# Optimization experiments

Measured on AMD Instinct MI355X. Metric: run time of the kernel, lower is better.

## Reference

```python
import jax, jax.numpy as jnp
import numpy as np

B, L, S, H, E = 2, 2048, 2048, 8, 64
MASK_SCALE = 10000.0
TAU_MIN, TAU_MAX = 0.1, 5.0
THR_MIN, THR_MAX = 0.01, 0.99


def setup_inputs() -> dict:
    key = jax.random.key(0)
    ks = jax.random.split(key, 7)
    query = jax.random.normal(ks[0], (B, L, H, E), jnp.float32)
    k_ = jax.random.normal(ks[1], (B, S, H, E), jnp.float32)
    value = jax.random.normal(ks[2], (B, S, H, E), jnp.float32)
    mask_miss_k = jnp.zeros((B, S), jnp.float32)  # unused in forward
    mask_miss_q = jnp.zeros((B, L), jnp.float32)  # unused in forward
    pos = jnp.arange(B * L, dtype=jnp.int32).reshape(B, L, 1)  # monotone positions per batch
    hard_mask = jax.random.randint(ks[3], (L, S), 0, 2, dtype=jnp.int32)
    hard_mask = hard_mask.at[jnp.arange(L), jnp.arange(S)].set(1)  # keep diagonal open
    # learned parameters / stochastic state
    phi = jax.random.normal(ks[4], (H, L, S), jnp.float32)  # DAG edge logits (per head)
    log_tau_gs = jnp.asarray(np.log(2.0), jnp.float32)
    threshold = jnp.asarray(0.5, jnp.float32)
    u = jax.random.uniform(ks[5], (H, L, S), jnp.float32, 1e-6, 1.0 - 1e-6)  # Gumbel base noise
    return {"query": query, "key": k_, "value": value, "mask_miss_k": mask_miss_k,
            "mask_miss_q": mask_miss_q, "pos": pos, "causal_mask": 1,
            "hard_mask": hard_mask, "phi": phi, "log_tau_gs": log_tau_gs,
            "threshold": threshold, "u": u}


def reference(query, key, value, mask_miss_k, mask_miss_q, pos, causal_mask,
              hard_mask, phi, log_tau_gs, threshold, u):
    e = query.shape[-1]
    scale = 1.0 / np.sqrt(e)
    # scores: (B, H, L, S)
    scores = jnp.einsum('blhe,bshe->bhls', query, key)
    if causal_mask:
        p = pos[..., 0]  # (B, L)
        causal = jnp.where(p[:, None, :] > p[:, :, None], -jnp.inf, 0.0).astype(scores.dtype)
        scores = scores + causal[:, None, :, :]
    # Gumbel-sigmoid relaxed DAG mask
    tau = jnp.clip(jnp.exp(log_tau_gs), TAU_MIN, TAU_MAX)
    gumbel = jnp.log(u + 1e-8) - jnp.log(1.0 - u + 1e-8)
    m_relaxed = jax.nn.sigmoid((gumbel + phi) / tau)  # (H, L, S)
    thr = jnp.clip(threshold, THR_MIN, THR_MAX)
    dag_add = MASK_SCALE * jnp.minimum(m_relaxed - thr, 0.0)  # <=0 additive penalty
    scores = scores + dag_add[None, :, :, :]
    # hard mask applied pre-softmax as -inf
    scores = jnp.where(hard_mask[None, None, :, :] == 0, -jnp.inf, scores)
    att = jax.nn.softmax(scale * scores, axis=-1)  # dropout p=0 (eval)
    out = jnp.einsum('bhls,bshe->blhe', att, value)  # (B, L, H, E)
    return out
```

## Files before the change

kernel.cpp:

```cpp
#include <hip/hip_runtime.h>


#define Bz 2
#define Lz 2048
#define Sz 2048
#define Hz 8
#define Ez 64
#define NSEG 4
#define NEG_BIG (-1e30f)

typedef __attribute__((ext_vector_type(8))) short short8;
typedef __attribute__((ext_vector_type(4))) short short4v;
typedef __attribute__((ext_vector_type(4))) float f32x4;

__device__ __forceinline__ float fast_rcp(float x) { return __builtin_amdgcn_rcpf(x); }

__device__ __forceinline__ short f2bf(float x) {
    unsigned bits = __builtin_bit_cast(unsigned, x);
    bits += 0x7FFFu + ((bits >> 16) & 1u);
    return (short)(bits >> 16);
}

__global__ void pack_qk(const float* __restrict__ q, const float* __restrict__ k,
                        short* __restrict__ qp, short* __restrict__ kp)
{
    const int t = blockIdx.x * 256 + threadIdx.x;
    const float4 qv = ((const float4*)q)[t];
    const float4 kv = ((const float4*)k)[t];
    const int e4   = t & 15;
    const int rest = t >> 4;
    const int h    = rest & 7;
    const int bl   = rest >> 3;
    const int b    = bl >> 11;
    const int l    = bl & 2047;
    const int o    = ((b*Hz + h)*Lz + l)*Ez + e4*4;
    short4v qo, ko;
    qo[0] = f2bf(qv.x*0.125f); qo[1] = f2bf(qv.y*0.125f);
    qo[2] = f2bf(qv.z*0.125f); qo[3] = f2bf(qv.w*0.125f);
    ko[0] = f2bf(kv.x); ko[1] = f2bf(kv.y); ko[2] = f2bf(kv.z); ko[3] = f2bf(kv.w);
    *(short4v*)&qp[o] = qo;
    *(short4v*)&kp[o] = ko;
}

__global__ void pack_vt(const float* __restrict__ v, short* __restrict__ vt)
{
    const int blk = blockIdx.x;
    const int st  = blk & 63;
    const int h   = (blk >> 6) & 7;
    const int b   = blk >> 9;
    const int s0  = st * 32;
    const int e   = threadIdx.x & 63;
    const int sc  = threadIdx.x >> 6;
    short8 ov;
#pragma unroll
    for (int j = 0; j < 8; ++j) {
        const int s = s0 + sc*8 + j;
        ov[j] = f2bf(v[((b*Sz + s)*Hz + h)*Ez + e]);
    }
    *(short8*)&vt[((b*Hz + h)*Ez + e)*Sz + s0 + sc*8] = ov;
}

__global__ __launch_bounds__(256, 2) void attn_main(
    const float* __restrict__ phi, const float* __restrict__ u,
    const int* __restrict__ hard_mask, const int* __restrict__ causal_p,
    const float* __restrict__ log_tau_p, const float* __restrict__ thr_p,
    const short* __restrict__ qp, const short* __restrict__ kp,
    const short* __restrict__ vt,
    float* __restrict__ Op, float* __restrict__ Mp, float* __restrict__ Lp)
{
    const int lane  = threadIdx.x & 63;
    const int wslot = threadIdx.x >> 6;
    const int wu    = blockIdx.x * 4 + wslot;
    const int seg   = wu & 3;
    const int qq    = wu >> 2;
    const int h     = qq & 7;
    const int c     = 127 - (qq >> 3);
    const int l_base = c * 16;
    const int ln    = lane & 15;
    const int quad  = lane >> 4;

    const int causal = *causal_p;
    float tau = __expf(*log_tau_p);
    tau = fminf(fmaxf(tau, 0.1f), 5.0f);
    const float inv_tau = 1.0f / tau;
    const float thr = fminf(fmaxf(*thr_p, 0.01f), 0.99f);

    short8 qf[2][2];
#pragma unroll
    for (int b = 0; b < 2; ++b)
#pragma unroll
        for (int k = 0; k < 2; ++k)
            qf[b][k] = *(const short8*)&qp[((b*Hz + h)*Lz + l_base + ln)*Ez + k*32 + quad*8];

    f32x4 O[2][4];
    float m_r[2][4], l_r[2][4];
#pragma unroll
    for (int b = 0; b < 2; ++b) {
#pragma unroll
        for (int ne = 0; ne < 4; ++ne) { f32x4 z = {0.f,0.f,0.f,0.f}; O[b][ne] = z; }
#pragma unroll
        for (int r = 0; r < 4; ++r) { m_r[b][r] = -INFINITY; l_r[b][r] = 0.f; }
    }

    const int T = causal ? (((l_base + 15) >> 6) + 1) : (Sz >> 6);

    __shared__ __align__(16) short plds[4][16*72];
    short* myp = &plds[wslot][0];

    for (int t = seg; t < T; t += NSEG) {
        const int s0 = t << 6;

        float dg[4][4];
#pragma unroll
        for (int nt = 0; nt < 4; ++nt) {
#pragma unroll
            for (int r = 0; r < 4; ++r) {
                const int l = l_base + quad*4 + r;
                const int s = s0 + nt*16 + ln;
                const int off = (h*Lz + l)*Sz + s;
                const float ph = phi[off];
                const float uv = u[off];
                const int   hm = hard_mask[l*Sz + s];
                const float g  = __logf((uv + 1e-8f) * fast_rcp(1.0f - uv + 1e-8f));
                const float z  = (g + ph) * inv_tau;
                const float sg = fast_rcp(1.0f + __expf(-z));
                const float d  = 1250.0f * fminf(sg - thr, 0.0f);
                const bool dead = (hm == 0) || (causal && (s > l));
                dg[nt][r] = dead ? -INFINITY : d;
            }
        }

#pragma unroll
        for (int b = 0; b < 2; ++b) {
            short8 kf[4][2];
#pragma unroll
            for (int nt = 0; nt < 4; ++nt)
#pragma unroll
                for (int k = 0; k < 2; ++k)
                    kf[nt][k] = *(const short8*)&kp[((b*Hz + h)*Sz + s0 + nt*16 + ln)*Ez + k*32 + quad*8];

            f32x4 Sc[4];
#pragma unroll
            for (int nt = 0; nt < 4; ++nt) {
                f32x4 z4 = {0.f,0.f,0.f,0.f};
                z4 = __builtin_amdgcn_mfma_f32_16x16x32_bf16(qf[b][0], kf[nt][0], z4, 0, 0, 0);
                Sc[nt] = __builtin_amdgcn_mfma_f32_16x16x32_bf16(qf[b][1], kf[nt][1], z4, 0, 0, 0);
            }

            float tv[4][4], mx[4];
#pragma unroll
            for (int r = 0; r < 4; ++r) mx[r] = -INFINITY;
#pragma unroll
            for (int nt = 0; nt < 4; ++nt)
#pragma unroll
                for (int r = 0; r < 4; ++r) {
                    const float val = Sc[nt][r] + dg[nt][r];
                    tv[nt][r] = val;
                    mx[r] = fmaxf(mx[r], val);
                }
#pragma unroll
            for (int r = 0; r < 4; ++r)
#pragma unroll
                for (int o = 1; o < 16; o <<= 1)
                    mx[r] = fmaxf(mx[r], __shfl_xor(mx[r], o, 16));

            float al[4], mn[4];
#pragma unroll
            for (int r = 0; r < 4; ++r) {
                mn[r] = fmaxf(m_r[b][r], mx[r]);
                al[r] = __expf(fmaxf(m_r[b][r], NEG_BIG) - fmaxf(mn[r], NEG_BIG));
                m_r[b][r] = mn[r];
            }

            float ps[4] = {0.f, 0.f, 0.f, 0.f};
#pragma unroll
            for (int nt = 0; nt < 4; ++nt)
#pragma unroll
                for (int r = 0; r < 4; ++r) {
                    const float p = __expf(tv[nt][r] - fmaxf(mn[r], NEG_BIG));
                    ps[r] += p;
                    myp[(quad*4 + r)*72 + nt*16 + ln] = f2bf(p);
                }
#pragma unroll
            for (int r = 0; r < 4; ++r) {
#pragma unroll
                for (int o = 1; o < 16; o <<= 1)
                    ps[r] += __shfl_xor(ps[r], o, 16);
                l_r[b][r] = l_r[b][r] * al[r] + ps[r];
            }
#pragma unroll
            for (int ne = 0; ne < 4; ++ne)
#pragma unroll
                for (int r = 0; r < 4; ++r)
                    O[b][ne][r] *= al[r];

            short8 pa[2];
#pragma unroll
            for (int k = 0; k < 2; ++k)
                pa[k] = *(const short8*)&myp[ln*72 + k*32 + quad*8];

#pragma unroll
            for (int ne = 0; ne < 4; ++ne) {
                const short8 v0 = *(const short8*)&vt[((b*Hz + h)*Ez + ne*16 + ln)*Sz + s0 + quad*8];
                const short8 v1 = *(const short8*)&vt[((b*Hz + h)*Ez + ne*16 + ln)*Sz + s0 + 32 + quad*8];
                O[b][ne] = __builtin_amdgcn_mfma_f32_16x16x32_bf16(pa[0], v0, O[b][ne], 0, 0, 0);
                O[b][ne] = __builtin_amdgcn_mfma_f32_16x16x32_bf16(pa[1], v1, O[b][ne], 0, 0, 0);
            }
        }
    }

#pragma unroll
    for (int b = 0; b < 2; ++b) {
#pragma unroll
        for (int ne = 0; ne < 4; ++ne)
#pragma unroll
            for (int r = 0; r < 4; ++r) {
                const int l = l_base + quad*4 + r;
                Op[(((seg*2 + b)*Hz + h)*Lz + l)*Ez + ne*16 + ln] = O[b][ne][r];
            }
        if (ln == 0) {
#pragma unroll
            for (int r = 0; r < 4; ++r) {
                const int l = l_base + quad*4 + r;
                Mp[((seg*2 + b)*Hz + h)*Lz + l] = m_r[b][r];
                Lp[((seg*2 + b)*Hz + h)*Lz + l] = l_r[b][r];
            }
        }
    }
}

__global__ void merge_k(const float* __restrict__ Op, const float* __restrict__ Mp,
                        const float* __restrict__ Lp, float* __restrict__ out)
{
    const int t = blockIdx.x * 256 + threadIdx.x;
    const int e4   = (t & 15) * 4;
    const int rest = t >> 4;
    const int h    = rest & 7;
    const int bl   = rest >> 3;
    const int b    = bl >> 11;
    const int l    = bl & 2047;

    float ms[NSEG], ls[NSEG], m = -INFINITY;
#pragma unroll
    for (int s = 0; s < NSEG; ++s) {
        const int idx = ((s*2 + b)*Hz + h)*Lz + l;
        ms[s] = Mp[idx];
        ls[s] = Lp[idx];
        m = fmaxf(m, ms[s]);
    }
    const float mg = fmaxf(m, NEG_BIG);
    float den = 0.f, a0 = 0.f, a1 = 0.f, a2 = 0.f, a3 = 0.f;
#pragma unroll
    for (int s = 0; s < NSEG; ++s) {
        const float w = __expf(fmaxf(ms[s], NEG_BIG) - mg);
        den += w * ls[s];
        const float4 ov = *(const float4*)&Op[(((s*2 + b)*Hz + h)*Lz + l)*Ez + e4];
        a0 += w * ov.x; a1 += w * ov.y; a2 += w * ov.z; a3 += w * ov.w;
    }
    const float rd = 1.0f / den;
    float4 res;
    res.x = a0 * rd; res.y = a1 * rd; res.z = a2 * rd; res.w = a3 * rd;
    *(float4*)&out[((b*Lz + l)*Hz + h)*Ez + e4] = res;
}

extern "C" void kernel_launch(void* const* d_in, const int* in_sizes, int n_in,
                              void* d_out, int out_size, void* d_ws, size_t ws_size,
                              hipStream_t stream)
{
    const float* q     = (const float*)d_in[0];
    const float* k     = (const float*)d_in[1];
    const float* v     = (const float*)d_in[2];
    const int*   caus  = (const int*)d_in[6];
    const int*   hm    = (const int*)d_in[7];
    const float* phi   = (const float*)d_in[8];
    const float* ltau  = (const float*)d_in[9];
    const float* thr   = (const float*)d_in[10];
    const float* u     = (const float*)d_in[11];

    char* ws = (char*)d_ws;
    short* qp = (short*)(ws);
    short* kp = (short*)(ws + (size_t)( 4u << 20));
    short* vt = (short*)(ws + (size_t)( 8u << 20));
    float* Op = (float*)(ws + (size_t)(12u << 20));
    float* Mp = (float*)(ws + (size_t)(44u << 20));
    float* Lp = (float*)(ws + (size_t)(44u << 20) + (512u << 10));

    pack_qk <<<2048, 256, 0, stream>>>(q, k, qp, kp);
    pack_vt <<<1024, 256, 0, stream>>>(v, vt);
    attn_main<<<1024, 256, 0, stream>>>(phi, u, hm, caus, ltau, thr, qp, kp, vt, Op, Mp, Lp);
    merge_k <<<2048, 256, 0, stream>>>(Op, Mp, Lp, (float*)d_out);
}
```

Baseline: 400.1 us.

## Split KV into 8 segments with in-block merge, bitpacked hard mask, prefetched phi/u

Raises the KV split from 4 to 8 segments per query tile and doubles the grid. Each block's four waves now combine their partials in shared memory, so only two partials per row reach global memory and the final merge reads half as much. The hard mask is packed into bits in a new pre-pass, and phi/u loads for the next tile are double-buffered into registers to hide their latency. The per-tile row-sum shuffles move to a single reduction after the loop. The cost is more register pressure from the prefetch buffers, an extra kernel launch, and extra shared memory plus a block barrier.

```diff
diff --git a/kernel.cpp b/kernel.cpp
--- a/kernel.cpp
+++ b/kernel.cpp
@@ -6,7 +6,6 @@
 #define Sz 2048
 #define Hz 8
 #define Ez 64
-#define NSEG 4
 #define NEG_BIG (-1e30f)
 
 typedef __attribute__((ext_vector_type(8))) short short8;
@@ -60,24 +59,40 @@
     *(short8*)&vt[((b*Hz + h)*Ez + e)*Sz + s0 + sc*8] = ov;
 }
 
+__global__ void pack_hm(const int* __restrict__ hm, unsigned* __restrict__ hmb)
+{
+    const int t = blockIdx.x * 256 + threadIdx.x;
+    const int4* src = (const int4*)hm + t*8;
+    unsigned w = 0;
+#pragma unroll
+    for (int i = 0; i < 8; ++i) {
+        const int4 v = src[i];
+        w |= (v.x != 0 ? 1u : 0u) << (i*4 + 0);
+        w |= (v.y != 0 ? 1u : 0u) << (i*4 + 1);
+        w |= (v.z != 0 ? 1u : 0u) << (i*4 + 2);
+        w |= (v.w != 0 ? 1u : 0u) << (i*4 + 3);
+    }
+    hmb[t] = w;
+}
+
 __global__ __launch_bounds__(256, 2) void attn_main(
     const float* __restrict__ phi, const float* __restrict__ u,
-    const int* __restrict__ hard_mask, const int* __restrict__ causal_p,
+    const unsigned* __restrict__ hmb, const int* __restrict__ causal_p,
     const float* __restrict__ log_tau_p, const float* __restrict__ thr_p,
     const short* __restrict__ qp, const short* __restrict__ kp,
     const short* __restrict__ vt,
-    float* __restrict__ Op, float* __restrict__ Mp, float* __restrict__ Lp)
-{
-    const int lane  = threadIdx.x & 63;
-    const int wslot = threadIdx.x >> 6;
-    const int wu    = blockIdx.x * 4 + wslot;
-    const int seg   = wu & 3;
-    const int qq    = wu >> 2;
-    const int h     = qq & 7;
-    const int c     = 127 - (qq >> 3);
-    const int l_base = c * 16;
-    const int ln    = lane & 15;
-    const int quad  = lane >> 4;
+    float* __restrict__ Og, float* __restrict__ Mg, float* __restrict__ Lg)
+{
+    const int lane    = threadIdx.x & 63;
+    const int wslot   = threadIdx.x >> 6;
+    const int h       = blockIdx.x & 7;
+    const int r2      = blockIdx.x >> 3;
+    const int segpair = r2 & 1;
+    const int c       = 127 - (r2 >> 1);
+    const int seg     = segpair*4 + wslot;
+    const int l_base  = c * 16;
+    const int ln      = lane & 15;
+    const int quad    = lane >> 4;
 
     const int causal = *causal_p;
     float tau = __expf(*log_tau_p);
@@ -104,59 +119,66 @@
 
     const int T = causal ? (((l_base + 15) >> 6) + 1) : (Sz >> 6);
 
-    __shared__ __align__(16) short plds[4][16*72];
-    short* myp = &plds[wslot][0];
-
-    for (int t = seg; t < T; t += NSEG) {
+    __shared__ __align__(16) short plds[4][2][16*72];
+
+    const int mbase = (h*Lz + l_base + quad*4)*Sz + ln;
+
+    auto ldmask = [&](int t, float (&P)[16], float (&U)[16]) {
+        const int o0 = mbase + (t << 6);
+#pragma unroll
+        for (int nt = 0; nt < 4; ++nt)
+#pragma unroll
+            for (int r = 0; r < 4; ++r) {
+                P[nt*4+r] = phi[o0 + r*Sz + nt*16];
+                U[nt*4+r] = u[o0 + r*Sz + nt*16];
+            }
+    };
+
+    auto process = [&](int t, const float (&P)[16], const float (&U)[16]) {
         const int s0 = t << 6;
-
-        float dg[4][4];
-#pragma unroll
-        for (int nt = 0; nt < 4; ++nt) {
+        unsigned long long hmr[4];
+#pragma unroll
+        for (int r = 0; r < 4; ++r)
+            hmr[r] = *(const unsigned long long*)&hmb[(l_base + quad*4 + r)*64 + (s0 >> 5)];
+
+        float dg[16];
+#pragma unroll
+        for (int nt = 0; nt < 4; ++nt)
 #pragma unroll
             for (int r = 0; r < 4; ++r) {
                 const int l = l_base + quad*4 + r;
                 const int s = s0 + nt*16 + ln;
-                const int off = (h*Lz + l)*Sz + s;
-                const float ph = phi[off];
-                const float uv = u[off];
-                const int   hm = hard_mask[l*Sz + s];
+                const float uv = U[nt*4+r];
                 const float g  = __logf((uv + 1e-8f) * fast_rcp(1.0f - uv + 1e-8f));
-                const float z  = (g + ph) * inv_tau;
+                const float z  = (g + P[nt*4+r]) * inv_tau;
                 const float sg = fast_rcp(1.0f + __expf(-z));
                 const float d  = 1250.0f * fminf(sg - thr, 0.0f);
-                const bool dead = (hm == 0) || (causal && (s > l));
-                dg[nt][r] = dead ? -INFINITY : d;
-            }
-        }
+                const bool open = (((hmr[r] >> (nt*16 + ln)) & 1ull) != 0ull)
+                                  && !(causal && (s > l));
+                dg[nt*4+r] = open ? d : -INFINITY;
+            }
 
 #pragma unroll
         for (int b = 0; b < 2; ++b) {
-            short8 kf[4][2];
+            f32x4 Sc[4];
+#pragma unroll
+            for (int nt = 0; nt < 4; ++nt) {
+                const short8 k0 = *(const short8*)&kp[((b*Hz + h)*Sz + s0 + nt*16 + ln)*Ez + quad*8];
+                const short8 k1 = *(const short8*)&kp[((b*Hz + h)*Sz + s0 + nt*16 + ln)*Ez + 32 + quad*8];
+                f32x4 z4 = {0.f,0.f,0.f,0.f};
+                z4 = __builtin_amdgcn_mfma_f32_16x16x32_bf16(qf[b][0], k0, z4, 0, 0, 0);
+                Sc[nt] = __builtin_amdgcn_mfma_f32_16x16x32_bf16(qf[b][1], k1, Sc[nt] = z4, 0, 0, 0);
+            }
+
+            float mx[4];
+#pragma unroll
+            for (int r = 0; r < 4; ++r) mx[r] = -INFINITY;
 #pragma unroll
             for (int nt = 0; nt < 4; ++nt)
 #pragma unroll
-                for (int k = 0; k < 2; ++k)
-                    kf[nt][k] = *(const short8*)&kp[((b*Hz + h)*Sz + s0 + nt*16 + ln)*Ez + k*32 + quad*8];
-
-            f32x4 Sc[4];
-#pragma unroll
-            for (int nt = 0; nt < 4; ++nt) {
-                f32x4 z4 = {0.f,0.f,0.f,0.f};
-                z4 = __builtin_amdgcn_mfma_f32_16x16x32_bf16(qf[b][0], kf[nt][0], z4, 0, 0, 0);
-                Sc[nt] = __builtin_amdgcn_mfma_f32_16x16x32_bf16(qf[b][1], kf[nt][1], z4, 0, 0, 0);
-            }
-
-            float tv[4][4], mx[4];
-#pragma unroll
-            for (int r = 0; r < 4; ++r) mx[r] = -INFINITY;
-#pragma unroll
-            for (int nt = 0; nt < 4; ++nt)
-#pragma unroll
                 for (int r = 0; r < 4; ++r) {
-                    const float val = Sc[nt][r] + dg[nt][r];
-                    tv[nt][r] = val;
-                    mx[r] = fmaxf(mx[r], val);
+                    Sc[nt][r] += dg[nt*4+r];
+                    mx[r] = fmaxf(mx[r], Sc[nt][r]);
                 }
 #pragma unroll
             for (int r = 0; r < 4; ++r)
@@ -164,73 +186,127 @@
                 for (int o = 1; o < 16; o <<= 1)
                     mx[r] = fmaxf(mx[r], __shfl_xor(mx[r], o, 16));
 
-            float al[4], mn[4];
+            float al[4];
 #pragma unroll
             for (int r = 0; r < 4; ++r) {
-                mn[r] = fmaxf(m_r[b][r], mx[r]);
-                al[r] = __expf(fmaxf(m_r[b][r], NEG_BIG) - fmaxf(mn[r], NEG_BIG));
-                m_r[b][r] = mn[r];
-            }
-
+                const float mn = fmaxf(m_r[b][r], mx[r]);
+                al[r] = __expf(fmaxf(m_r[b][r], NEG_BIG) - fmaxf(mn, NEG_BIG));
+                m_r[b][r] = mn;
+            }
+
+            short* myp = &plds[wslot][b][0];
             float ps[4] = {0.f, 0.f, 0.f, 0.f};
 #pragma unroll
             for (int nt = 0; nt < 4; ++nt)
 #pragma unroll
                 for (int r = 0; r < 4; ++r) {
-                    const float p = __expf(tv[nt][r] - fmaxf(mn[r], NEG_BIG));
+                    const float p = __expf(Sc[nt][r] - fmaxf(m_r[b][r], NEG_BIG));
                     ps[r] += p;
                     myp[(quad*4 + r)*72 + nt*16 + ln] = f2bf(p);
                 }
 #pragma unroll
-            for (int r = 0; r < 4; ++r) {
-#pragma unroll
-                for (int o = 1; o < 16; o <<= 1)
-                    ps[r] += __shfl_xor(ps[r], o, 16);
+            for (int r = 0; r < 4; ++r)
                 l_r[b][r] = l_r[b][r] * al[r] + ps[r];
-            }
 #pragma unroll
             for (int ne = 0; ne < 4; ++ne)
 #pragma unroll
                 for (int r = 0; r < 4; ++r)
                     O[b][ne][r] *= al[r];
 
-            short8 pa[2];
-#pragma unroll
-            for (int k = 0; k < 2; ++k)
-                pa[k] = *(const short8*)&myp[ln*72 + k*32 + quad*8];
-
+            const short8 pa0 = *(const short8*)&myp[ln*72 + quad*8];
+            const short8 pa1 = *(const short8*)&myp[ln*72 + 32 + quad*8];
 #pragma unroll
             for (int ne = 0; ne < 4; ++ne) {
                 const short8 v0 = *(const short8*)&vt[((b*Hz + h)*Ez + ne*16 + ln)*Sz + s0 + quad*8];
                 const short8 v1 = *(const short8*)&vt[((b*Hz + h)*Ez + ne*16 + ln)*Sz + s0 + 32 + quad*8];
-                O[b][ne] = __builtin_amdgcn_mfma_f32_16x16x32_bf16(pa[0], v0, O[b][ne], 0, 0, 0);
-                O[b][ne] = __builtin_amdgcn_mfma_f32_16x16x32_bf16(pa[1], v1, O[b][ne], 0, 0, 0);
+                O[b][ne] = __builtin_amdgcn_mfma_f32_16x16x32_bf16(pa0, v0, O[b][ne], 0, 0, 0);
+                O[b][ne] = __builtin_amdgcn_mfma_f32_16x16x32_bf16(pa1, v1, O[b][ne], 0, 0, 0);
             }
         }
-    }
-
+    };
+
+    float PA[16], UA[16], PB[16], UB[16];
+    int t = seg;
+    if (t < T) ldmask(t, PA, UA);
+    int parity = 0;
+    for (; t < T; t += 8, parity ^= 1) {
+        if (parity == 0) {
+            if (t + 8 < T) ldmask(t + 8, PB, UB);
+            process(t, PA, UA);
+        } else {
+            if (t + 8 < T) ldmask(t + 8, PA, UA);
+            process(t, PB, UB);
+        }
+    }
+
+#pragma unroll
+    for (int b = 0; b < 2; ++b)
+#pragma unroll
+        for (int r = 0; r < 4; ++r) {
+            float lv = l_r[b][r];
+#pragma unroll
+            for (int o = 1; o < 16; o <<= 1) lv += __shfl_xor(lv, o, 16);
+            l_r[b][r] = lv;
+        }
+
+    __shared__ float oslab[4][2][16][64];
+    __shared__ float mslab[4][2][16];
+    __shared__ float lslab[4][2][16];
 #pragma unroll
     for (int b = 0; b < 2; ++b) {
 #pragma unroll
         for (int ne = 0; ne < 4; ++ne)
 #pragma unroll
+            for (int r = 0; r < 4; ++r)
+                oslab[wslot][b][quad*4 + r][ne*16 + ln] = O[b][ne][r];
+        if (ln == 0) {
+#pragma unroll
             for (int r = 0; r < 4; ++r) {
-                const int l = l_base + quad*4 + r;
-                Op[(((seg*2 + b)*Hz + h)*Lz + l)*Ez + ne*16 + ln] = O[b][ne][r];
-            }
-        if (ln == 0) {
-#pragma unroll
-            for (int r = 0; r < 4; ++r) {
-                const int l = l_base + quad*4 + r;
-                Mp[((seg*2 + b)*Hz + h)*Lz + l] = m_r[b][r];
-                Lp[((seg*2 + b)*Hz + h)*Lz + l] = l_r[b][r];
+                mslab[wslot][b][quad*4 + r] = m_r[b][r];
+                lslab[wslot][b][quad*4 + r] = l_r[b][r];
             }
         }
     }
-}
-
-__global__ void merge_k(const float* __restrict__ Op, const float* __restrict__ Mp,
-                        const float* __restrict__ Lp, float* __restrict__ out)
+    __syncthreads();
+
+    const int tb   = threadIdx.x >> 7;
+    const int trow = (threadIdx.x >> 3) & 15;
+    const int teg  = threadIdx.x & 7;
+    float mM = -INFINITY;
+#pragma unroll
+    for (int w = 0; w < 4; ++w) mM = fmaxf(mM, mslab[w][tb][trow]);
+    const float mMg = fmaxf(mM, NEG_BIG);
+    float wgt[4]; float lsum = 0.f;
+#pragma unroll
+    for (int w = 0; w < 4; ++w) {
+        wgt[w] = __expf(fmaxf(mslab[w][tb][trow], NEG_BIG) - mMg);
+        lsum += wgt[w] * lslab[w][tb][trow];
+    }
+    float acc[8];
+#pragma unroll
+    for (int e = 0; e < 8; ++e) acc[e] = 0.f;
+#pragma unroll
+    for (int w = 0; w < 4; ++w)
+#pragma unroll
+        for (int e = 0; e < 8; ++e)
+            acc[e] += wgt[w] * oslab[w][tb][trow][teg*8 + e];
+
+    const int lrow = l_base + trow;
+    const int oidx = (((segpair*2 + tb)*Hz + h)*Lz + lrow)*Ez + teg*8;
+    float4 o0, o1;
+    o0.x = acc[0]; o0.y = acc[1]; o0.z = acc[2]; o0.w = acc[3];
+    o1.x = acc[4]; o1.y = acc[5]; o1.z = acc[6]; o1.w = acc[7];
+    *(float4*)&Og[oidx]     = o0;
+    *(float4*)&Og[oidx + 4] = o1;
+    if (teg == 0) {
+        const int midx = ((segpair*2 + tb)*Hz + h)*Lz + lrow;
+        Mg[midx] = mM;
+        Lg[midx] = lsum;
+    }
+}
+
+__global__ void merge2(const float* __restrict__ Og, const float* __restrict__ Mg,
+                       const float* __restrict__ Lg, float* __restrict__ out)
 {
     const int t = blockIdx.x * 256 + threadIdx.x;
     const int e4   = (t & 15) * 4;
@@ -240,26 +316,23 @@
     const int b    = bl >> 11;
     const int l    = bl & 2047;
 
-    float ms[NSEG], ls[NSEG], m = -INFINITY;
-#pragma unroll
-    for (int s = 0; s < NSEG; ++s) {
-        const int idx = ((s*2 + b)*Hz + h)*Lz + l;
-        ms[s] = Mp[idx];
-        ls[s] = Lp[idx];
-        m = fmaxf(m, ms[s]);
-    }
+    const int i0 = ((0*2 + b)*Hz + h)*Lz + l;
+    const int i1 = ((1*2 + b)*Hz + h)*Lz + l;
+    const float m0 = Mg[i0], m1 = Mg[i1];
+    const float l0 = Lg[i0], l1 = Lg[i1];
+    const float m  = fmaxf(m0, m1);
     const float mg = fmaxf(m, NEG_BIG);
-    float den = 0.f, a0 = 0.f, a1 = 0.f, a2 = 0.f, a3 = 0.f;
-#pragma unroll
-    for (int s = 0; s < NSEG; ++s) {
-        const float w = __expf(fmaxf(ms[s], NEG_BIG) - mg);
-        den += w * ls[s];
-        const float4 ov = *(const float4*)&Op[(((s*2 + b)*Hz + h)*Lz + l)*Ez + e4];
-        a0 += w * ov.x; a1 += w * ov.y; a2 += w * ov.z; a3 += w * ov.w;
-    }
-    const float rd = 1.0f / den;
+    const float w0 = __expf(fmaxf(m0, NEG_BIG) - mg);
+    const float w1 = __expf(fmaxf(m1, NEG_BIG) - mg);
+    const float den = w0*l0 + w1*l1;
+    const float rd  = 1.0f / den;
+    const float4 a = *(const float4*)&Og[i0*Ez + e4];
+    const float4 c = *(const float4*)&Og[i1*Ez + e4];
     float4 res;
-    res.x = a0 * rd; res.y = a1 * rd; res.z = a2 * rd; res.w = a3 * rd;
+    res.x = (w0*a.x + w1*c.x) * rd;
+    res.y = (w0*a.y + w1*c.y) * rd;
+    res.z = (w0*a.z + w1*c.z) * rd;
+    res.w = (w0*a.w + w1*c.w) * rd;
     *(float4*)&out[((b*Lz + l)*Hz + h)*Ez + e4] = res;
 }
 
@@ -267,26 +340,28 @@
                               void* d_out, int out_size, void* d_ws, size_t ws_size,
                               hipStream_t stream)
 {
-    const float* q     = (const float*)d_in[0];
-    const float* k     = (const float*)d_in[1];
-    const float* v     = (const float*)d_in[2];
-    const int*   caus  = (const int*)d_in[6];
-    const int*   hm    = (const int*)d_in[7];
-    const float* phi   = (const float*)d_in[8];
-    const float* ltau  = (const float*)d_in[9];
-    const float* thr   = (const float*)d_in[10];
-    const float* u     = (const float*)d_in[11];
+    const float* q    = (const float*)d_in[0];
+    const float* k    = (const float*)d_in[1];
+    const float* v    = (const float*)d_in[2];
+    const int*   caus = (const int*)d_in[6];
+    const int*   hm   = (const int*)d_in[7];
+    const float* phi  = (const float*)d_in[8];
+    const float* ltau = (const float*)d_in[9];
+    const float* thr  = (const float*)d_in[10];
+    const float* u    = (const float*)d_in[11];
 
     char* ws = (char*)d_ws;
-    short* qp = (short*)(ws);
-    short* kp = (short*)(ws + (size_t)( 4u << 20));
-    short* vt = (short*)(ws + (size_t)( 8u << 20));
-    float* Op = (float*)(ws + (size_t)(12u << 20));
-    float* Mp = (float*)(ws + (size_t)(44u << 20));
-    float* Lp = (float*)(ws + (size_t)(44u << 20) + (512u << 10));
+    short*    qp  = (short*)   (ws);
+    short*    kp  = (short*)   (ws + (size_t)( 4u << 20));
+    short*    vt  = (short*)   (ws + (size_t)( 8u << 20));
+    unsigned* hmb = (unsigned*)(ws + (size_t)(12u << 20));
+    float*    Og  = (float*)   (ws + (size_t)(13u << 20));
+    float*    Mg  = (float*)   (ws + (size_t)(29u << 20));
+    float*    Lg  = (float*)   (ws + (size_t)(29u << 20) + (256u << 10));
 
     pack_qk <<<2048, 256, 0, stream>>>(q, k, qp, kp);
     pack_vt <<<1024, 256, 0, stream>>>(v, vt);
-    attn_main<<<1024, 256, 0, stream>>>(phi, u, hm, caus, ltau, thr, qp, kp, vt, Op, Mp, Lp);
-    merge_k <<<2048, 256, 0, stream>>>(Op, Mp, Lp, (float*)d_out);
-}
+    pack_hm <<< 512, 256, 0, stream>>>(hm, hmb);
+    attn_main<<<2048, 256, 0, stream>>>(phi, u, hmb, caus, ltau, thr, qp, kp, vt, Og, Mg, Lg);
+    merge2  <<<2048, 256, 0, stream>>>(Og, Mg, Lg, (float*)d_out);
+}
```

Result: no change. 404.4 us (+1.1%).

## Precompute bf16 DAG mask with row-max shift, drop online softmax and merge kernel

Applied to the files above, without the earlier changes.

Adds a mask kernel that computes the Gumbel-sigmoid DAG penalty once per (h,l,s), takes its row maximum over open entries, and stores the shifted penalty as bf16 in a causal-packed tile layout. Because QK scores are tiny next to the penalty scale, the attention kernel uses this fixed shift as a stable max and skips online-softmax rescaling. It also splits the key range across 8 waves of one block per (b,h,chunk) and merges them in shared memory, so the separate merge kernel and its partial-output traffic go away. The costs are two passes over phi/u in the mask kernel, a bf16 round-trip for the penalty, and reliance on scores staying small for exp to stay in range.

```diff
diff --git a/kernel.cpp b/kernel.cpp
--- a/kernel.cpp
+++ b/kernel.cpp
@@ -6,8 +6,6 @@
 #define Sz 2048
 #define Hz 8
 #define Ez 64
-#define NSEG 4
-#define NEG_BIG (-1e30f)
 
 typedef __attribute__((ext_vector_type(8))) short short8;
 typedef __attribute__((ext_vector_type(4))) short short4v;
@@ -19,6 +17,12 @@
     unsigned bits = __builtin_bit_cast(unsigned, x);
     bits += 0x7FFFu + ((bits >> 16) & 1u);
     return (short)(bits >> 16);
+}
+
+__device__ __forceinline__ int tile_base_of_chunk(int c, int causal) {
+    if (!causal) return c * 32;
+    const int g = c >> 2, r = c & 3;
+    return 2*g*(g-1) + g*r + c;
 }
 
 __global__ void pack_qk(const float* __restrict__ q, const float* __restrict__ k,
@@ -60,233 +64,219 @@
     *(short8*)&vt[((b*Hz + h)*Ez + e)*Sz + s0 + sc*8] = ov;
 }
 
-__global__ __launch_bounds__(256, 2) void attn_main(
+__global__ __launch_bounds__(256) void mask_k(
     const float* __restrict__ phi, const float* __restrict__ u,
-    const int* __restrict__ hard_mask, const int* __restrict__ causal_p,
+    const int* __restrict__ hm, const int* __restrict__ causal_p,
     const float* __restrict__ log_tau_p, const float* __restrict__ thr_p,
-    const short* __restrict__ qp, const short* __restrict__ kp,
-    const short* __restrict__ vt,
-    float* __restrict__ Op, float* __restrict__ Mp, float* __restrict__ Lp)
-{
-    const int lane  = threadIdx.x & 63;
-    const int wslot = threadIdx.x >> 6;
-    const int wu    = blockIdx.x * 4 + wslot;
-    const int seg   = wu & 3;
-    const int qq    = wu >> 2;
-    const int h     = qq & 7;
-    const int c     = 127 - (qq >> 3);
-    const int l_base = c * 16;
-    const int ln    = lane & 15;
-    const int quad  = lane >> 4;
-
+    unsigned short* __restrict__ dag)
+{
+    const int h = blockIdx.x & 7;
+    const int c = 127 - (blockIdx.x >> 3);
     const int causal = *causal_p;
     float tau = __expf(*log_tau_p);
     tau = fminf(fmaxf(tau, 0.1f), 5.0f);
     const float inv_tau = 1.0f / tau;
     const float thr = fminf(fmaxf(*thr_p, 0.01f), 0.99f);
 
-    short8 qf[2][2];
-#pragma unroll
-    for (int b = 0; b < 2; ++b)
-#pragma unroll
-        for (int k = 0; k < 2; ++k)
-            qf[b][k] = *(const short8*)&qp[((b*Hz + h)*Lz + l_base + ln)*Ez + k*32 + quad*8];
-
-    f32x4 O[2][4];
-    float m_r[2][4], l_r[2][4];
-#pragma unroll
-    for (int b = 0; b < 2; ++b) {
-#pragma unroll
-        for (int ne = 0; ne < 4; ++ne) { f32x4 z = {0.f,0.f,0.f,0.f}; O[b][ne] = z; }
-#pragma unroll
-        for (int r = 0; r < 4; ++r) { m_r[b][r] = -INFINITY; l_r[b][r] = 0.f; }
-    }
-
-    const int T = causal ? (((l_base + 15) >> 6) + 1) : (Sz >> 6);
-
-    __shared__ __align__(16) short plds[4][16*72];
-    short* myp = &plds[wslot][0];
-
-    for (int t = seg; t < T; t += NSEG) {
-        const int s0 = t << 6;
-
-        float dg[4][4];
+    const int T   = causal ? ((c >> 2) + 1) : 32;
+    const int row = threadIdx.x >> 4;
+    const int sc4 = (threadIdx.x & 15) * 4;
+    const int l   = c*16 + row;
+    const float* prow = &phi[(h*Lz + l)*Sz];
+    const float* urow = &u[(h*Lz + l)*Sz];
+    const int*   hrow = &hm[l*Sz];
+
+    float md = -INFINITY;
+    for (int t = 0; t < T; ++t) {
+        const int s = t*64 + sc4;
+        const float4 ph = *(const float4*)&prow[s];
+        const float4 uv = *(const float4*)&urow[s];
+        const int4   hv = *(const int4*)&hrow[s];
+        const float pa[4] = {ph.x, ph.y, ph.z, ph.w};
+        const float ua[4] = {uv.x, uv.y, uv.z, uv.w};
+        const int   ha[4] = {hv.x, hv.y, hv.z, hv.w};
+#pragma unroll
+        for (int j = 0; j < 4; ++j) {
+            const float g  = __logf((ua[j] + 1e-8f) * fast_rcp(1.0f - ua[j] + 1e-8f));
+            const float z  = (g + pa[j]) * inv_tau;
+            const float sg = fast_rcp(1.0f + __expf(-z));
+            const float d  = 1250.0f * fminf(sg - thr, 0.0f);
+            const bool open = (ha[j] != 0) && !(causal && (s + j > l));
+            if (open) md = fmaxf(md, d);
+        }
+    }
+#pragma unroll
+    for (int o = 1; o < 16; o <<= 1)
+        md = fmaxf(md, __shfl_xor(md, o, 16));
+
+    const int hstride = causal ? 2112 : 4096;
+    unsigned short* dbase = dag + (h*hstride + tile_base_of_chunk(c, causal))*1024
+                                + row*64 + sc4;
+    for (int t = T - 1; t >= 0; --t) {
+        const int s = t*64 + sc4;
+        const float4 ph = *(const float4*)&prow[s];
+        const float4 uv = *(const float4*)&urow[s];
+        const int4   hv = *(const int4*)&hrow[s];
+        const float pa[4] = {ph.x, ph.y, ph.z, ph.w};
+        const float ua[4] = {uv.x, uv.y, uv.z, uv.w};
+        const int   ha[4] = {hv.x, hv.y, hv.z, hv.w};
+        unsigned short o4[4];
+#pragma unroll
+        for (int j = 0; j < 4; ++j) {
+            const float g  = __logf((ua[j] + 1e-8f) * fast_rcp(1.0f - ua[j] + 1e-8f));
+            const float z  = (g + pa[j]) * inv_tau;
+            const float sg = fast_rcp(1.0f + __expf(-z));
+            const float d  = 1250.0f * fminf(sg - thr, 0.0f);
+            const bool open = (ha[j] != 0) && !(causal && (s + j > l));
+            o4[j] = open ? (unsigned short)f2bf(d - md) : (unsigned short)0xFF80u;
+        }
+        unsigned short* dst = dbase + t*1024;
+        dst[0] = o4[0]; dst[1] = o4[1]; dst[2] = o4[2]; dst[3] = o4[3];
+    }
+}
+
+__global__ __launch_bounds__(512, 4) void attn_main(
+    const unsigned short* __restrict__ dag, const int* __restrict__ causal_p,
+    const short* __restrict__ qp, const short* __restrict__ kp,
+    const short* __restrict__ vt, float* __restrict__ out)
+{
+    const int lane = threadIdx.x & 63;
+    const int seg  = threadIdx.x >> 6;
+    const int h    = blockIdx.x & 7;
+    const int b    = (blockIdx.x >> 3) & 1;
+    const int c    = 127 - (blockIdx.x >> 4);
+    const int l_base = c * 16;
+    const int ln   = lane & 15;
+    const int quad = lane >> 4;
+
+    const int causal = *causal_p;
+    const int T = causal ? ((c >> 2) + 1) : 32;
+    const int hstride = causal ? 2112 : 4096;
+    const unsigned short* dbase = dag + (h*hstride + tile_base_of_chunk(c, causal))*1024
+                                      + (quad*4)*64 + ln;
+
+    short8 qf[2];
+#pragma unroll
+    for (int k = 0; k < 2; ++k)
+        qf[k] = *(const short8*)&qp[((b*Hz + h)*Lz + l_base + ln)*Ez + k*32 + quad*8];
+
+    f32x4 O[4];
+    float l_r[4];
+#pragma unroll
+    for (int ne = 0; ne < 4; ++ne) { f32x4 z = {0.f,0.f,0.f,0.f}; O[ne] = z; }
+#pragma unroll
+    for (int r = 0; r < 4; ++r) l_r[r] = 0.f;
+
+    __shared__ __align__(16) char shm[8 * 4608];
+    __shared__ float lslab[8][16];
+    short* myp = (short*)(shm + seg*4608);
+
+    auto lddag = [&](int t, unsigned (&D)[16]) {
+        const unsigned short* dp = dbase + t*1024;
+#pragma unroll
+        for (int nt = 0; nt < 4; ++nt)
+#pragma unroll
+            for (int r = 0; r < 4; ++r)
+                D[nt*4+r] = dp[r*64 + nt*16];
+    };
+
+    auto process = [&](int t, const unsigned (&D)[16]) {
+        const short* kbase = &kp[((b*Hz + h)*Sz + t*64 + ln)*Ez + quad*8];
+        f32x4 Sc[4];
 #pragma unroll
         for (int nt = 0; nt < 4; ++nt) {
+            const short8 k0 = *(const short8*)&kbase[nt*16*Ez];
+            const short8 k1 = *(const short8*)&kbase[nt*16*Ez + 32];
+            f32x4 z4 = {0.f,0.f,0.f,0.f};
+            z4 = __builtin_amdgcn_mfma_f32_16x16x32_bf16(qf[0], k0, z4, 0, 0, 0);
+            Sc[nt] = __builtin_amdgcn_mfma_f32_16x16x32_bf16(qf[1], k1, z4, 0, 0, 0);
+        }
+#pragma unroll
+        for (int nt = 0; nt < 4; ++nt)
 #pragma unroll
             for (int r = 0; r < 4; ++r) {
-                const int l = l_base + quad*4 + r;
-                const int s = s0 + nt*16 + ln;
-                const int off = (h*Lz + l)*Sz + s;
-                const float ph = phi[off];
-                const float uv = u[off];
-                const int   hm = hard_mask[l*Sz + s];
-                const float g  = __logf((uv + 1e-8f) * fast_rcp(1.0f - uv + 1e-8f));
-                const float z  = (g + ph) * inv_tau;
-                const float sg = fast_rcp(1.0f + __expf(-z));
-                const float d  = 1250.0f * fminf(sg - thr, 0.0f);
-                const bool dead = (hm == 0) || (causal && (s > l));
-                dg[nt][r] = dead ? -INFINITY : d;
+                const float dg = __builtin_bit_cast(float, D[nt*4+r] << 16);
+                const float p  = __expf(Sc[nt][r] + dg);
+                l_r[r] += p;
+                myp[(quad*4 + r)*72 + nt*16 + ln] = f2bf(p);
             }
-        }
-
-#pragma unroll
-        for (int b = 0; b < 2; ++b) {
-            short8 kf[4][2];
-#pragma unroll
-            for (int nt = 0; nt < 4; ++nt)
-#pragma unroll
-                for (int k = 0; k < 2; ++k)
-                    kf[nt][k] = *(const short8*)&kp[((b*Hz + h)*Sz + s0 + nt*16 + ln)*Ez + k*32 + quad*8];
-
-            f32x4 Sc[4];
-#pragma unroll
-            for (int nt = 0; nt < 4; ++nt) {
-                f32x4 z4 = {0.f,0.f,0.f,0.f};
-                z4 = __builtin_amdgcn_mfma_f32_16x16x32_bf16(qf[b][0], kf[nt][0], z4, 0, 0, 0);
-                Sc[nt] = __builtin_amdgcn_mfma_f32_16x16x32_bf16(qf[b][1], kf[nt][1], z4, 0, 0, 0);
-            }
-
-            float tv[4][4], mx[4];
-#pragma unroll
-            for (int r = 0; r < 4; ++r) mx[r] = -INFINITY;
-#pragma unroll
-            for (int nt = 0; nt < 4; ++nt)
-#pragma unroll
-                for (int r = 0; r < 4; ++r) {
-                    const float val = Sc[nt][r] + dg[nt][r];
-                    tv[nt][r] = val;
-                    mx[r] = fmaxf(mx[r], val);
-                }
-#pragma unroll
-            for (int r = 0; r < 4; ++r)
-#pragma unroll
-                for (int o = 1; o < 16; o <<= 1)
-                    mx[r] = fmaxf(mx[r], __shfl_xor(mx[r], o, 16));
-
-            float al[4], mn[4];
-#pragma unroll
-            for (int r = 0; r < 4; ++r) {
-                mn[r] = fmaxf(m_r[b][r], mx[r]);
-                al[r] = __expf(fmaxf(m_r[b][r], NEG_BIG) - fmaxf(mn[r], NEG_BIG));
-                m_r[b][r] = mn[r];
-            }
-
-            float ps[4] = {0.f, 0.f, 0.f, 0.f};
-#pragma unroll
-            for (int nt = 0; nt < 4; ++nt)
-#pragma unroll
-                for (int r = 0; r < 4; ++r) {
-                    const float p = __expf(tv[nt][r] - fmaxf(mn[r], NEG_BIG));
-                    ps[r] += p;
-                    myp[(quad*4 + r)*72 + nt*16 + ln] = f2bf(p);
-                }
-#pragma unroll
-            for (int r = 0; r < 4; ++r) {
-#pragma unroll
-                for (int o = 1; o < 16; o <<= 1)
-                    ps[r] += __shfl_xor(ps[r], o, 16);
-                l_r[b][r] = l_r[b][r] * al[r] + ps[r];
-            }
-#pragma unroll
-            for (int ne = 0; ne < 4; ++ne)
-#pragma unroll
-                for (int r = 0; r < 4; ++r)
-                    O[b][ne][r] *= al[r];
-
-            short8 pa[2];
-#pragma unroll
-            for (int k = 0; k < 2; ++k)
-                pa[k] = *(const short8*)&myp[ln*72 + k*32 + quad*8];
-
-#pragma unroll
-            for (int ne = 0; ne < 4; ++ne) {
-                const short8 v0 = *(const short8*)&vt[((b*Hz + h)*Ez + ne*16 + ln)*Sz + s0 + quad*8];
-                const short8 v1 = *(const short8*)&vt[((b*Hz + h)*Ez + ne*16 + ln)*Sz + s0 + 32 + quad*8];
-                O[b][ne] = __builtin_amdgcn_mfma_f32_16x16x32_bf16(pa[0], v0, O[b][ne], 0, 0, 0);
-                O[b][ne] = __builtin_amdgcn_mfma_f32_16x16x32_bf16(pa[1], v1, O[b][ne], 0, 0, 0);
-            }
-        }
-    }
-
-#pragma unroll
-    for (int b = 0; b < 2; ++b) {
-#pragma unroll
-        for (int ne = 0; ne < 4; ++ne)
-#pragma unroll
-            for (int r = 0; r < 4; ++r) {
-                const int l = l_base + quad*4 + r;
-                Op[(((seg*2 + b)*Hz + h)*Lz + l)*Ez + ne*16 + ln] = O[b][ne][r];
-            }
-        if (ln == 0) {
-#pragma unroll
-            for (int r = 0; r < 4; ++r) {
-                const int l = l_base + quad*4 + r;
-                Mp[((seg*2 + b)*Hz + h)*Lz + l] = m_r[b][r];
-                Lp[((seg*2 + b)*Hz + h)*Lz + l] = l_r[b][r];
-            }
-        }
-    }
-}
-
-__global__ void merge_k(const float* __restrict__ Op, const float* __restrict__ Mp,
-                        const float* __restrict__ Lp, float* __restrict__ out)
-{
-    const int t = blockIdx.x * 256 + threadIdx.x;
-    const int e4   = (t & 15) * 4;
-    const int rest = t >> 4;
-    const int h    = rest & 7;
-    const int bl   = rest >> 3;
-    const int b    = bl >> 11;
-    const int l    = bl & 2047;
-
-    float ms[NSEG], ls[NSEG], m = -INFINITY;
-#pragma unroll
-    for (int s = 0; s < NSEG; ++s) {
-        const int idx = ((s*2 + b)*Hz + h)*Lz + l;
-        ms[s] = Mp[idx];
-        ls[s] = Lp[idx];
-        m = fmaxf(m, ms[s]);
-    }
-    const float mg = fmaxf(m, NEG_BIG);
-    float den = 0.f, a0 = 0.f, a1 = 0.f, a2 = 0.f, a3 = 0.f;
-#pragma unroll
-    for (int s = 0; s < NSEG; ++s) {
-        const float w = __expf(fmaxf(ms[s], NEG_BIG) - mg);
-        den += w * ls[s];
-        const float4 ov = *(const float4*)&Op[(((s*2 + b)*Hz + h)*Lz + l)*Ez + e4];
-        a0 += w * ov.x; a1 += w * ov.y; a2 += w * ov.z; a3 += w * ov.w;
+        const short8 pa0 = *(const short8*)&myp[ln*72 + quad*8];
+        const short8 pa1 = *(const short8*)&myp[ln*72 + 32 + quad*8];
+        const short* vb = &vt[((b*Hz + h)*Ez + ln)*Sz + t*64 + quad*8];
+#pragma unroll
+        for (int ne = 0; ne < 4; ++ne) {
+            const short8 v0 = *(const short8*)&vb[ne*16*Sz];
+            const short8 v1 = *(const short8*)&vb[ne*16*Sz + 32];
+            O[ne] = __builtin_amdgcn_mfma_f32_16x16x32_bf16(pa0, v0, O[ne], 0, 0, 0);
+            O[ne] = __builtin_amdgcn_mfma_f32_16x16x32_bf16(pa1, v1, O[ne], 0, 0, 0);
+        }
+    };
+
+    unsigned DA[16], DB[16];
+    int t = seg;
+    if (t < T) lddag(t, DA);
+    int parity = 0;
+    for (; t < T; t += 8, parity ^= 1) {
+        if (!parity) { if (t + 8 < T) lddag(t + 8, DB); process(t, DA); }
+        else         { if (t + 8 < T) lddag(t + 8, DA); process(t, DB); }
+    }
+
+#pragma unroll
+    for (int r = 0; r < 4; ++r) {
+        float lv = l_r[r];
+#pragma unroll
+        for (int o = 1; o < 16; o <<= 1) lv += __shfl_xor(lv, o, 16);
+        l_r[r] = lv;
+    }
+    float* fo = (float*)(shm + seg*4608);
+#pragma unroll
+    for (int ne = 0; ne < 4; ++ne)
+#pragma unroll
+        for (int r = 0; r < 4; ++r)
+            fo[(quad*4 + r)*64 + ne*16 + ln] = O[ne][r];
+    if (ln == 0) {
+#pragma unroll
+        for (int r = 0; r < 4; ++r) lslab[seg][quad*4 + r] = l_r[r];
+    }
+    __syncthreads();
+
+    const int row = threadIdx.x >> 5;
+    const int e   = (threadIdx.x & 31) * 2;
+    float den = 0.f, a0 = 0.f, a1 = 0.f;
+#pragma unroll
+    for (int w = 0; w < 8; ++w) {
+        den += lslab[w][row];
+        const float* fw = (const float*)(shm + w*4608) + row*64 + e;
+        a0 += fw[0];
+        a1 += fw[1];
     }
     const float rd = 1.0f / den;
-    float4 res;
-    res.x = a0 * rd; res.y = a1 * rd; res.z = a2 * rd; res.w = a3 * rd;
-    *(float4*)&out[((b*Lz + l)*Hz + h)*Ez + e4] = res;
+    float2 res; res.x = a0 * rd; res.y = a1 * rd;
+    *(float2*)&out[((b*Lz + l_base + row)*Hz + h)*Ez + e] = res;
 }
 
 extern "C" void kernel_launch(void* const* d_in, const int* in_sizes, int n_in,
                               void* d_out, int out_size, void* d_ws, size_t ws_size,
                               hipStream_t stream)
 {
-    const float* q     = (const float*)d_in[0];
-    const float* k     = (const float*)d_in[1];
-    const float* v     = (const float*)d_in[2];
-    const int*   caus  = (const int*)d_in[6];
-    const int*   hm    = (const int*)d_in[7];
-    const float* phi   = (const float*)d_in[8];
-    const float* ltau  = (const float*)d_in[9];
-    const float* thr   = (const float*)d_in[10];
-    const float* u     = (const float*)d_in[11];
+    const float* q    = (const float*)d_in[0];
+    const float* k    = (const float*)d_in[1];
+    const float* v    = (const float*)d_in[2];
+    const int*   caus = (const int*)d_in[6];
+    const int*   hm   = (const int*)d_in[7];
+    const float* phi  = (const float*)d_in[8];
+    const float* ltau = (const float*)d_in[9];
+    const float* thr  = (const float*)d_in[10];
+    const float* u    = (const float*)d_in[11];
 
     char* ws = (char*)d_ws;
-    short* qp = (short*)(ws);
-    short* kp = (short*)(ws + (size_t)( 4u << 20));
-    short* vt = (short*)(ws + (size_t)( 8u << 20));
-    float* Op = (float*)(ws + (size_t)(12u << 20));
-    float* Mp = (float*)(ws + (size_t)(44u << 20));
-    float* Lp = (float*)(ws + (size_t)(44u << 20) + (512u << 10));
+    short*          qp  = (short*)(ws);
+    short*          kp  = (short*)(ws + (size_t)( 4u << 20));
+    short*          vt  = (short*)(ws + (size_t)( 8u << 20));
+    unsigned short* dag = (unsigned short*)(ws + (size_t)(12u << 20));
 
     pack_qk <<<2048, 256, 0, stream>>>(q, k, qp, kp);
     pack_vt <<<1024, 256, 0, stream>>>(v, vt);
-    attn_main<<<1024, 256, 0, stream>>>(phi, u, hm, caus, ltau, thr, qp, kp, vt, Op, Mp, Lp);
-    merge_k <<<2048, 256, 0, stream>>>(Op, Mp, Lp, (float*)d_out);
-}
+    mask_k  <<<1024, 256, 0, stream>>>(phi, u, hm, caus, ltau, thr, dag);
+    attn_main<<<2048, 512, 0, stream>>>(dag, caus, qp, kp, vt, (float*)d_out);
+}
```

Result: slower. 424.3 us (+6.0%).
